# Kernel tuning notes

Hardware: AMD Instinct MI355X
Metric: run time of the kernel (lower is better)

## Reference

```python
import jax, jax.numpy as jnp
import numpy as np
import math

N_HEADS = 4
N_ITERS = 2  # SSFormer n=2; each loop iteration recomputes the same values (no feedback in the original code)
BN_EPS = 1e-5


def _attention(q, k, v):
    """SSTransformer: multi-head cross-attention over flattened spatial dims.
    q,k,v: [B, C, H, W] -> returns [B, C, L] with L = H*W.
    """
    b, c = q.shape[0], q.shape[1]
    L = q.shape[2] * q.shape[3]
    ch = c // N_HEADS
    scale = 1.0 / math.sqrt(math.sqrt(ch))
    qf = (q.reshape(b * N_HEADS, ch, L) * scale)
    kf = (k.reshape(b * N_HEADS, ch, L) * scale)
    vf = v.reshape(b * N_HEADS, ch, L)
    # weight: [B*H, t, s]
    w = jnp.einsum('bct,bcs->bts', qf, kf)
    w = jax.nn.softmax(w.astype(jnp.float32), axis=-1).astype(w.dtype)
    a = jnp.einsum('bts,bcs->bct', w, vf)
    return a.reshape(b, c, L)


def setup_inputs() -> dict:
    key = jax.random.key(0)
    k1, k2, k3, k4 = jax.random.split(key, 4)
    B, C, H, W = 8, 512, 32, 32
    c = jax.random.normal(k1, (B, C, H, W), dtype=jnp.float32)
    e = jax.random.normal(k2, (B, C, H, W), dtype=jnp.float32)
    conv_w = jax.random.normal(k3, (C, C, 1, 1), dtype=jnp.float32) / math.sqrt(C)
    conv_b = jax.random.normal(k4, (C,), dtype=jnp.float32) * 0.02
    bn_gamma = jnp.ones((C,), dtype=jnp.float32)
    bn_beta = jnp.zeros((C,), dtype=jnp.float32)
    return {"c": c, "e": e, "conv_w": conv_w, "conv_b": conv_b,
            "bn_gamma": bn_gamma, "bn_beta": bn_beta}


def reference(c, e, conv_w, conv_b, bn_gamma, bn_beta):
    bs, ch, h, w = c.shape
    L = h * w
    for _ in range(N_ITERS):
        _c = _attention(e, c, c)                       # [B, C, L]
        _e = _attention(_c.reshape(bs, ch, h, w), e, e)  # [B, C, L]
    _e = _e.reshape(bs, ch, h, w)
    # Proj: 1x1 conv + BatchNorm2d (training-mode batch stats) + Swish
    x = jnp.einsum('oc,bchw->bohw', conv_w.reshape(ch, ch), _e) + conv_b[None, :, None, None]
    mean = jnp.mean(x, axis=(0, 2, 3), keepdims=True)
    var = jnp.var(x, axis=(0, 2, 3), keepdims=True)
    xn = (x - mean) * jax.lax.rsqrt(var + BN_EPS)
    xn = xn * bn_gamma[None, :, None, None] + bn_beta[None, :, None, None]
    return xn * jax.nn.sigmoid(xn)
```

## Files before the change

### kernel.cpp

```cpp
#include <hip/hip_runtime.h>
#include <hip/hip_bf16.h>

typedef __attribute__((ext_vector_type(8))) short short8;
typedef __attribute__((ext_vector_type(4))) float floatx4;
typedef __attribute__((ext_vector_type(4))) float f32x4;
typedef __attribute__((ext_vector_type(16))) float f32x16;
typedef unsigned short u16;
typedef unsigned int u32;
typedef __attribute__((ext_vector_type(4))) unsigned int u32x4;
typedef __attribute__((ext_vector_type(8))) unsigned short ushort8;

#define LSEQ 1024
#define CHD  128
#define CEXP 0.12751744900425577f
#define THR_RAW 62.73318f

static __device__ __forceinline__ float b2f(u16 u) {
  union { u32 i; float f; } x; x.i = ((u32)u) << 16; return x.f;
}
static __device__ __forceinline__ u32 cvtpk(float a, float b) {
  u32 r;
  asm("v_cvt_pk_bf16_f32 %0, %1, %2" : "=v"(r) : "v"(a), "v"(b));
  return r;
}
static __device__ __forceinline__ void swap32(u32& a, u32& b) {
  asm("v_permlane32_swap_b32 %0, %1" : "+v"(a), "+v"(b));
}
static __device__ __forceinline__ short8 mk8(u32 a, u32 b, u32 c, u32 d) {
  union { u32x4 u; short8 s; } x;
  x.u[0] = a; x.u[1] = b; x.u[2] = c; x.u[3] = d;
  return x.s;
}
static __device__ __forceinline__ float exp2f_fast(float x) {
  float r;
  asm("v_exp_f32 %0, %1" : "=v"(r) : "v"(x));
  return r;
}
static __device__ __forceinline__ void gl_lds16(const void* g, void* l) {
  __builtin_amdgcn_global_load_lds((__attribute__((address_space(1))) const void*)g,
                                   (__attribute__((address_space(3))) void*)l, 16, 0, 0);
}
#define BARRIER() do { asm volatile("" ::: "memory"); __builtin_amdgcn_s_barrier(); asm volatile("" ::: "memory"); } while (0)
#define LGKMW()   do { asm volatile("s_waitcnt lgkmcnt(0)" ::: "memory"); } while (0)

__global__ __launch_bounds__(256) void k_prep(const float* __restrict__ cin,
                                              const float* __restrict__ ein,
                                              const float* __restrict__ Wf,
                                              u16* __restrict__ cV, u16* __restrict__ cT,
                                              u16* __restrict__ eV, u16* __restrict__ eT,
                                              u16* __restrict__ wb) {
  __shared__ u16 tile[32][72];
  int z = blockIdx.z;
  int tid = threadIdx.x;
  if (z >= 64) {
    int wblk = (z - 64) * 64 + blockIdx.y * 16 + blockIdx.x;
    int base = (wblk * 256 + tid) * 8;
    f32x4 a = *(const f32x4*)(Wf + base);
    f32x4 b = *(const f32x4*)(Wf + base + 4);
    u32x4 u;
    u[0] = cvtpk(a[0], a[1]); u[1] = cvtpk(a[2], a[3]);
    u[2] = cvtpk(b[0], b[1]); u[3] = cvtpk(b[2], b[3]);
    *(u32x4*)(wb + base) = u;
    return;
  }
  const float* in = (z < 32) ? cin : ein;
  u16* outV = (z < 32) ? cV : eV;
  u16* outT = (z < 32) ? cT : eT;
  int bh = z & 31, c0 = blockIdx.y * 32, s0 = blockIdx.x * 64;
  int cl = tid >> 3, sc = tid & 7;
  size_t off = ((size_t)bh * CHD + c0 + cl) * LSEQ + s0 + sc * 8;
  f32x4 a = *(const f32x4*)(in + off);
  f32x4 b = *(const f32x4*)(in + off + 4);
  u32x4 u;
  u[0] = cvtpk(a[0], a[1]); u[1] = cvtpk(a[2], a[3]);
  u[2] = cvtpk(b[0], b[1]); u[3] = cvtpk(b[2], b[3]);
  *(u32x4*)(outV + off) = u;
  *(u32x4*)&tile[cl][sc * 8] = u;
  __syncthreads();
  int sl = tid >> 2, cc = tid & 3;
  ushort8 v;
#pragma unroll
  for (int j = 0; j < 8; ++j) v[j] = tile[cc * 8 + j][sl];
  *(ushort8*)(outT + ((size_t)bh * LSEQ + s0 + sl) * CHD + c0 + cc * 8) = v;
}

__global__ __launch_bounds__(256, 2) void k_attn(const u16* __restrict__ eT,
                                                 const u16* __restrict__ cT,
                                                 const u16* __restrict__ cV,
                                                 const u16* __restrict__ eV,
                                                 u16* __restrict__ outT) {
  __shared__ char ldsbuf[66560];

  int bh = blockIdx.x, tt = blockIdx.y;
  int tid = threadIdx.x;
  int w = tid >> 6, lane = tid & 63;
  int tw = w & 1, sw = w >> 1;
  int ln = lane & 31, h = lane >> 5;
  int t0 = tt * 64 + tw * 32;

  float* bmbuf = (float*)(ldsbuf + 65536);
  float* lbuf  = (float*)(ldsbuf + 65536 + 512);

  auto stageK = [&](int buf, int sb, const char* kTb) {
#pragma unroll
    for (int it = 0; it < 4; ++it) {
      int bb = it * 4096 + tid * 16;
      int row = bb >> 8;
      int cb = (bb & 255) ^ ((row & 15) << 4);
      gl_lds16(kTb + (size_t)(sb * 64 + row) * 256 + cb, ldsbuf + buf * 16384 + bb);
    }
  };
  auto stageV = [&](int buf, int sb, const char* vb) {
#pragma unroll
    for (int it = 0; it < 4; ++it) {
      int bb = it * 4096 + tid * 16;
      int row = bb >> 7;
      int cb = (bb & 127) ^ ((row & 7) << 4);
      gl_lds16(vb + (size_t)row * 2048 + sb * 128 + cb, ldsbuf + 32768 + buf * 16384 + bb);
    }
  };

  short8 bq[8];
  f32x16 oacc[4];
  float m_r, l_r;
  int swz = (ln & 7) << 4;
  int kswz = (ln & 15) << 4;
  int krow = sw * 32 + ln;

  auto flash = [&](const char* kTb, const char* vb) {
    m_r = -1e30f; l_r = 0.f;
#pragma unroll
    for (int i = 0; i < 4; ++i)
#pragma unroll
      for (int r = 0; r < 16; ++r) oacc[i][r] = 0.f;

    stageK(0, 0, kTb); stageV(0, 0, vb);
    asm volatile("s_waitcnt vmcnt(0)" ::: "memory");
    BARRIER();

    for (int sb = 0; sb < 16; ++sb) {
      int cur = sb & 1;
      const char* K = ldsbuf + cur * 16384;
      const char* V = ldsbuf + 32768 + cur * 16384;
      f32x16 sa;
#pragma unroll
      for (int r = 0; r < 16; ++r) sa[r] = 0.f;

      if (sb < 15) stageK(cur ^ 1, sb + 1, kTb);
      short8 ka0 = *(const short8*)(K + krow * 256 + ((0  + h * 16) ^ kswz));
      short8 ka1 = *(const short8*)(K + krow * 256 + ((32 + h * 16) ^ kswz));
      short8 ka2 = *(const short8*)(K + krow * 256 + ((64 + h * 16) ^ kswz));
      short8 ka3 = *(const short8*)(K + krow * 256 + ((96 + h * 16) ^ kswz));
      BARRIER();
      __builtin_amdgcn_s_setprio(1);
      sa = __builtin_amdgcn_mfma_f32_32x32x16_bf16(ka0, bq[0], sa, 0, 0, 0);
      sa = __builtin_amdgcn_mfma_f32_32x32x16_bf16(ka1, bq[1], sa, 0, 0, 0);
      sa = __builtin_amdgcn_mfma_f32_32x32x16_bf16(ka2, bq[2], sa, 0, 0, 0);
      sa = __builtin_amdgcn_mfma_f32_32x32x16_bf16(ka3, bq[3], sa, 0, 0, 0);
      __builtin_amdgcn_s_setprio(0);
      BARRIER();

      if (sb < 15) stageV(cur ^ 1, sb + 1, vb);
      short8 kb0 = *(const short8*)(K + krow * 256 + ((128 + h * 16) ^ kswz));
      short8 kb1 = *(const short8*)(K + krow * 256 + ((160 + h * 16) ^ kswz));
      short8 kb2 = *(const short8*)(K + krow * 256 + ((192 + h * 16) ^ kswz));
      short8 kb3 = *(const short8*)(K + krow * 256 + ((224 + h * 16) ^ kswz));
      BARRIER();
      __builtin_amdgcn_s_setprio(1);
      sa = __builtin_amdgcn_mfma_f32_32x32x16_bf16(kb0, bq[4], sa, 0, 0, 0);
      sa = __builtin_amdgcn_mfma_f32_32x32x16_bf16(kb1, bq[5], sa, 0, 0, 0);
      sa = __builtin_amdgcn_mfma_f32_32x32x16_bf16(kb2, bq[6], sa, 0, 0, 0);
      sa = __builtin_amdgcn_mfma_f32_32x32x16_bf16(kb3, bq[7], sa, 0, 0, 0);
      __builtin_amdgcn_s_setprio(0);
      BARRIER();

      float bm = fmaxf(fmaxf(sa[0], sa[1]), fmaxf(sa[2], sa[3]));
      bm = fmaxf(bm, fmaxf(fmaxf(sa[4], sa[5]), fmaxf(sa[6], sa[7])));
      bm = fmaxf(bm, fmaxf(fmaxf(sa[8], sa[9]), fmaxf(sa[10], sa[11])));
      bm = fmaxf(bm, fmaxf(fmaxf(sa[12], sa[13]), fmaxf(sa[14], sa[15])));
      bm = fmaxf(bm, __shfl_xor(bm, 32));
      if (lane < 32) bmbuf[(tw * 2 + sw) * 32 + lane] = bm;
      LGKMW();
      BARRIER();
      bm = fmaxf(bm, bmbuf[(tw * 2 + (sw ^ 1)) * 32 + ln]);
      bool stay = __all(bm - m_r <= THR_RAW);
      if (!stay) {
        float mn = fmaxf(m_r, bm);
        float corr = exp2f_fast((m_r - mn) * CEXP);
        m_r = mn; l_r *= corr;
#pragma unroll
        for (int i = 0; i < 4; ++i)
#pragma unroll
          for (int r = 0; r < 16; ++r) oacc[i][r] *= corr;
      }
      float mnC = m_r * CEXP;
      float rs = 0.f;
#pragma unroll
      for (int r = 0; r < 16; ++r) {
        float p = exp2f_fast(__builtin_fmaf(sa[r], CEXP, -mnC));
        sa[r] = p; rs += p;
      }
      rs += __shfl_xor(rs, 32);
      l_r += rs;

      short8 bp0, bp1;
      {
        u32 w0 = cvtpk(sa[0], sa[1]),  w1 = cvtpk(sa[2], sa[3]);
        u32 w2 = cvtpk(sa[4], sa[5]),  w3 = cvtpk(sa[6], sa[7]);
        swap32(w0, w2); swap32(w1, w3);
        bp0 = mk8(w0, w1, w2, w3);
        u32 w4 = cvtpk(sa[8], sa[9]),  w5 = cvtpk(sa[10], sa[11]);
        u32 w6 = cvtpk(sa[12], sa[13]), w7 = cvtpk(sa[14], sa[15]);
        swap32(w4, w6); swap32(w5, w7);
        bp1 = mk8(w4, w5, w6, w7);
      }

      int vc0 = sw * 64 + h * 16;
      short8 va0 = *(const short8*)(V + (0  + ln) * 128 + (vc0 ^ swz));
      short8 va1 = *(const short8*)(V + (32 + ln) * 128 + (vc0 ^ swz));
      short8 va2 = *(const short8*)(V + (64 + ln) * 128 + (vc0 ^ swz));
      short8 va3 = *(const short8*)(V + (96 + ln) * 128 + (vc0 ^ swz));
      BARRIER();
      __builtin_amdgcn_s_setprio(1);
      oacc[0] = __builtin_amdgcn_mfma_f32_32x32x16_bf16(va0, bp0, oacc[0], 0, 0, 0);
      oacc[1] = __builtin_amdgcn_mfma_f32_32x32x16_bf16(va1, bp0, oacc[1], 0, 0, 0);
      oacc[2] = __builtin_amdgcn_mfma_f32_32x32x16_bf16(va2, bp0, oacc[2], 0, 0, 0);
      oacc[3] = __builtin_amdgcn_mfma_f32_32x32x16_bf16(va3, bp0, oacc[3], 0, 0, 0);
      __builtin_amdgcn_s_setprio(0);
      BARRIER();

      int vc1 = sw * 64 + 32 + h * 16;
      short8 vb0 = *(const short8*)(V + (0  + ln) * 128 + (vc1 ^ swz));
      short8 vb1 = *(const short8*)(V + (32 + ln) * 128 + (vc1 ^ swz));
      short8 vb2 = *(const short8*)(V + (64 + ln) * 128 + (vc1 ^ swz));
      short8 vb3 = *(const short8*)(V + (96 + ln) * 128 + (vc1 ^ swz));
      BARRIER();
      __builtin_amdgcn_s_setprio(1);
      oacc[0] = __builtin_amdgcn_mfma_f32_32x32x16_bf16(vb0, bp1, oacc[0], 0, 0, 0);
      oacc[1] = __builtin_amdgcn_mfma_f32_32x32x16_bf16(vb1, bp1, oacc[1], 0, 0, 0);
      oacc[2] = __builtin_amdgcn_mfma_f32_32x32x16_bf16(vb2, bp1, oacc[2], 0, 0, 0);
      oacc[3] = __builtin_amdgcn_mfma_f32_32x32x16_bf16(vb3, bp1, oacc[3], 0, 0, 0);
      __builtin_amdgcn_s_setprio(0);
      asm volatile("s_waitcnt vmcnt(0)" ::: "memory");
      BARRIER();
    }
  };

  auto merge_sw = [&]() {
    float* mb = (float*)(ldsbuf + 32768 + tw * 16384);
    if (sw == 1) {
#pragma unroll
      for (int i = 0; i < 4; ++i)
#pragma unroll
        for (int r = 0; r < 16; ++r) mb[(i * 16 + r) * 64 + lane] = oacc[i][r];
      if (lane < 32) lbuf[tw * 32 + lane] = l_r;
    }
    LGKMW();
    BARRIER();
    if (sw == 0) {
#pragma unroll
      for (int i = 0; i < 4; ++i)
#pragma unroll
        for (int r = 0; r < 16; ++r) oacc[i][r] += mb[(i * 16 + r) * 64 + lane];
      l_r += lbuf[tw * 32 + ln];
    }
  };

  const u16* qbase = eT + ((size_t)bh * LSEQ + t0 + ln) * CHD + h * 8;
#pragma unroll
  for (int k = 0; k < 8; ++k) bq[k] = *(const short8*)(qbase + k * 16);

  flash((const char*)(cT + (size_t)bh * LSEQ * CHD),
        (const char*)(cV + (size_t)bh * CHD * LSEQ));

  merge_sw();
  if (sw == 0) {
    float inv = 1.0f / l_r;
    char* qt = ldsbuf + tw * 8192;
#pragma unroll
    for (int m = 0; m < 4; ++m)
#pragma unroll
      for (int q = 0; q < 8; ++q) {
        u32 pk = cvtpk(oacc[m][2 * q] * inv, oacc[m][2 * q + 1] * inv);
        int c2 = m * 64 + 4 * (q & 1) + 16 * (q >> 1) + 8 * h;
        *(u32*)(qt + ln * 256 + (c2 ^ swz)) = pk;
      }
  }
  LGKMW();
  BARRIER();
  {
    const char* qt = ldsbuf + tw * 8192;
#pragma unroll
    for (int k = 0; k < 8; ++k)
      bq[k] = *(const short8*)(qt + ln * 256 + ((k * 32 + h * 16) ^ swz));
  }
  LGKMW();
  BARRIER();

  flash((const char*)(eT + (size_t)bh * LSEQ * CHD),
        (const char*)(eV + (size_t)bh * CHD * LSEQ));

  merge_sw();
  BARRIER();
  if (sw == 0) {
    float inv = 1.0f / l_r;
    char* ot = ldsbuf + tw * 8192;
#pragma unroll
    for (int m = 0; m < 4; ++m)
#pragma unroll
      for (int q = 0; q < 8; ++q) {
        u32 pk = cvtpk(oacc[m][2 * q] * inv, oacc[m][2 * q + 1] * inv);
        int c2 = m * 64 + 4 * (q & 1) + 16 * (q >> 1) + 8 * h;
        *(u32*)(ot + ln * 256 + (c2 ^ swz)) = pk;
      }
    asm volatile("" ::: "memory");
    u16* orow = outT + ((size_t)bh * LSEQ + t0 + ln) * CHD;
#pragma unroll
    for (int it = 0; it < 8; ++it) {
      int col = h * 128 + it * 16;
      ushort8 d = *(const ushort8*)(ot + ln * 256 + (col ^ swz));
      *(ushort8*)((char*)orow + col) = d;
    }
  }
}

__global__ __launch_bounds__(256) void k_proj(const u16* __restrict__ Wm,
                                              const u16* __restrict__ eT,
                                              const float* __restrict__ bias,
                                              u16* __restrict__ x,
                                              float* __restrict__ pstat) {
  __shared__ char lds[65536];
  int lt = blockIdx.x, ot = blockIdx.y;
  int b = lt >> 3;
  int l0b = (lt & 7) * 128;
  int o0 = ot * 128;
  int tid = threadIdx.x, w = tid >> 6, lane = tid & 63, lo = lane & 15, hi = lane >> 4;
  int wm = w >> 1, wn = w & 1;
  const char* Wb = (const char*)Wm;
  const char* eTb = (const char*)eT;

  auto stageA = [&](int buf, int kb) {
    char* dst = lds + buf * 16384;
#pragma unroll
    for (int it = 0; it < 4; ++it) {
      int bb = it * 4096 + tid * 16;
      int row = bb >> 7;
      int cb = (bb & 127) ^ ((row & 7) << 4);
      gl_lds16(Wb + (size_t)(o0 + row) * 1024 + kb * 128 + cb, dst + bb);
    }
  };
  auto stageB = [&](int buf, int kb) {
    char* dst = lds + 32768 + buf * 16384;
    int page = b * 4 + (kb >> 1);
    int choff = (kb & 1) * 128;
#pragma unroll
    for (int it = 0; it < 4; ++it) {
      int bb = it * 4096 + tid * 16;
      int row = bb >> 7;
      int cb = (bb & 127) ^ ((row & 7) << 4);
      gl_lds16(eTb + ((size_t)page * 1024 + l0b + row) * 256 + choff + cb, dst + bb);
    }
  };

  floatx4 acc[4][4];
#pragma unroll
  for (int i = 0; i < 4; ++i)
#pragma unroll
    for (int j = 0; j < 4; ++j) { acc[i][j][0]=0.f; acc[i][j][1]=0.f; acc[i][j][2]=0.f; acc[i][j][3]=0.f; }

  stageA(0, 0); stageB(0, 0);

  for (int kb = 0; kb < 8; ++kb) {
    int cur = kb & 1;
    __builtin_amdgcn_s_barrier();
    if (kb < 7) { stageA(cur ^ 1, kb + 1); stageB(cur ^ 1, kb + 1); }
    if (kb < 7) { asm volatile("s_waitcnt vmcnt(8)" ::: "memory"); }
    else        { asm volatile("s_waitcnt vmcnt(0)" ::: "memory"); }
    __builtin_amdgcn_s_barrier();
    const char* A = lds + cur * 16384;
    const char* B = lds + 32768 + cur * 16384;
#pragma unroll
    for (int kk = 0; kk < 2; ++kk) {
      short8 af[4], bf[4];
#pragma unroll
      for (int mi = 0; mi < 4; ++mi) {
        int row = wm * 64 + mi * 16 + lo;
        af[mi] = *(const short8*)(A + row * 128 + ((kk * 64 + hi * 16) ^ ((row & 7) << 4)));
      }
#pragma unroll
      for (int ni = 0; ni < 4; ++ni) {
        int row = wn * 64 + ni * 16 + lo;
        bf[ni] = *(const short8*)(B + row * 128 + ((kk * 64 + hi * 16) ^ ((row & 7) << 4)));
      }
      __builtin_amdgcn_s_setprio(1);
#pragma unroll
      for (int mi = 0; mi < 4; ++mi)
#pragma unroll
        for (int ni = 0; ni < 4; ++ni)
          acc[mi][ni] = __builtin_amdgcn_mfma_f32_16x16x32_bf16(af[mi], bf[ni], acc[mi][ni], 0, 0, 0);
      __builtin_amdgcn_s_setprio(0);
    }
  }

  int prow = lt * 2 + wn;
#pragma unroll
  for (int mi = 0; mi < 4; ++mi) {
#pragma unroll
    for (int r = 0; r < 4; ++r) {
      int o = o0 + wm * 64 + mi * 16 + hi * 4 + r;
      float bv = bias[o];
      float s = 0.f, q = 0.f;
#pragma unroll
      for (int ni = 0; ni < 4; ++ni) {
        float xv = acc[mi][ni][r] + bv;
        x[((size_t)b * 512 + o) * LSEQ + l0b + wn * 64 + ni * 16 + lo] = cvtpk(xv, xv) & 0xffff;
        s += xv; q += xv * xv;
      }
#pragma unroll
      for (int d = 1; d < 16; d <<= 1) { s += __shfl_xor(s, d); q += __shfl_xor(q, d); }
      if (lo == 0) {
        pstat[(size_t)prow * 512 + o] = s;
        pstat[65536 + (size_t)prow * 512 + o] = q;
      }
    }
  }
}

__global__ __launch_bounds__(256) void k_final(const u16* __restrict__ x,
                                               const float* __restrict__ pstat,
                                               const float* __restrict__ gamma,
                                               const float* __restrict__ beta,
                                               float* __restrict__ out) {
  __shared__ float sscale[2], sshift[2];
  int bid = blockIdx.x;
  int tid = threadIdx.x;
  if (tid < 128) {
    int k = tid >> 6;
    int chn = (bid * 2 + k) & 511;
    int l = tid & 63;
    float s = pstat[(size_t)l * 512 + chn] + pstat[(size_t)(l + 64) * 512 + chn];
    float q = pstat[65536 + (size_t)l * 512 + chn] + pstat[65536 + (size_t)(l + 64) * 512 + chn];
#pragma unroll
    for (int d = 1; d < 64; d <<= 1) { s += __shfl_xor(s, d); q += __shfl_xor(q, d); }
    if (l == 0) {
      const float invn = 1.0f / 8192.0f;
      float mean = s * invn;
      float var = q * invn - mean * mean;
      float rstd = rsqrtf(var + 1e-5f);
      float g = gamma[chn] * rstd;
      sscale[k] = g;
      sshift[k] = beta[chn] - mean * g;
    }
  }
  __syncthreads();
  int base = (bid * 256 + tid) * 8;
  int k2 = tid >> 7;
  float sc = sscale[k2], sh = sshift[k2];
  ushort8 vx = *(const ushort8*)(x + base);
  f32x4 o0, o1;
#pragma unroll
  for (int j = 0; j < 8; ++j) {
    float xn = b2f(vx[j]) * sc + sh;
    float sg = 1.0f / (1.0f + __expf(-xn));
    float r = xn * sg;
    if (j < 4) o0[j] = r; else o1[j - 4] = r;
  }
  *(f32x4*)(out + base) = o0;
  *(f32x4*)(out + base + 4) = o1;
}

extern "C" void kernel_launch(void* const* d_in, const int* in_sizes, int n_in,
                              void* d_out, int out_size, void* d_ws, size_t ws_size,
                              hipStream_t stream) {
  const float* c     = (const float*)d_in[0];
  const float* e     = (const float*)d_in[1];
  const float* Wf    = (const float*)d_in[2];
  const float* bias  = (const float*)d_in[3];
  const float* gamma = (const float*)d_in[4];
  const float* beta  = (const float*)d_in[5];
  float* outp = (float*)d_out;

  char* ws = (char*)d_ws;
  const size_t TB = (size_t)32 * 1024 * 128 * 2;
  u16* eT  = (u16*)(ws);
  u16* cT  = (u16*)(ws + TB);
  u16* cV  = (u16*)(ws + 2 * TB);
  u16* eV  = (u16*)(ws + 3 * TB);
  u16* xT  = (u16*)(ws + 4 * TB);
  u16* Wbf = (u16*)(ws + 5 * TB);
  float* pstat = (float*)(ws + 5 * TB + (2 << 20));
  u16* x   = (u16*)(ws + 6 * TB);

  dim3 tb(256);

  k_prep<<<dim3(16, 4, 66), tb, 0, stream>>>(c, e, Wf, cV, cT, eV, eT, Wbf);
  k_attn<<<dim3(32, 16), tb, 0, stream>>>(eT, cT, cV, eV, xT);
  k_proj<<<dim3(64, 4), tb, 0, stream>>>(Wbf, xT, bias, x, pstat);
  k_final<<<dim3(2048), tb, 0, stream>>>(x, pstat, gamma, beta, outp);
}
```

Baseline: 93.38 us.

## Load K directly into registers with prefetch and cut per-step barriers

K tiles now bypass LDS: each thread reads its own K fragments from global memory into registers and prefetches the next block's fragments while the current block is processed. V stays staged in LDS, with a partial vmcnt wait so the prefetched K loads can remain in flight. Several barriers around the QK and PV MFMA groups are removed and one is added before the merge. The cost is more VGPRs for the kc/kn arrays, which may hurt occupancy under launch_bounds(256,2), plus uncoalesced direct global reads of K.

```diff
diff --git a/kernel.cpp b/kernel.cpp
--- a/kernel.cpp
+++ b/kernel.cpp
@@ -101,15 +101,6 @@
   float* bmbuf = (float*)(ldsbuf + 65536);
   float* lbuf  = (float*)(ldsbuf + 65536 + 512);
 
-  auto stageK = [&](int buf, int sb, const char* kTb) {
-#pragma unroll
-    for (int it = 0; it < 4; ++it) {
-      int bb = it * 4096 + tid * 16;
-      int row = bb >> 8;
-      int cb = (bb & 255) ^ ((row & 15) << 4);
-      gl_lds16(kTb + (size_t)(sb * 64 + row) * 256 + cb, ldsbuf + buf * 16384 + bb);
-    }
-  };
   auto stageV = [&](int buf, int sb, const char* vb) {
 #pragma unroll
     for (int it = 0; it < 4; ++it) {
@@ -124,7 +115,6 @@
   f32x16 oacc[4];
   float m_r, l_r;
   int swz = (ln & 7) << 4;
-  int kswz = (ln & 15) << 4;
   int krow = sw * 32 + ln;
 
   auto flash = [&](const char* kTb, const char* vb) {
@@ -134,45 +124,36 @@
 #pragma unroll
       for (int r = 0; r < 16; ++r) oacc[i][r] = 0.f;
 
-    stageK(0, 0, kTb); stageV(0, 0, vb);
+    short8 kn[8], kc[8];
+    {
+      const char* kb = kTb + (size_t)krow * 256 + h * 16;
+#pragma unroll
+      for (int k = 0; k < 8; ++k) kn[k] = *(const short8*)(kb + k * 32);
+    }
+    stageV(0, 0, vb);
     asm volatile("s_waitcnt vmcnt(0)" ::: "memory");
     BARRIER();
 
     for (int sb = 0; sb < 16; ++sb) {
       int cur = sb & 1;
-      const char* K = ldsbuf + cur * 16384;
       const char* V = ldsbuf + 32768 + cur * 16384;
+
+#pragma unroll
+      for (int k = 0; k < 8; ++k) kc[k] = kn[k];
+
       f32x16 sa;
 #pragma unroll
       for (int r = 0; r < 16; ++r) sa[r] = 0.f;
-
-      if (sb < 15) stageK(cur ^ 1, sb + 1, kTb);
-      short8 ka0 = *(const short8*)(K + krow * 256 + ((0  + h * 16) ^ kswz));
-      short8 ka1 = *(const short8*)(K + krow * 256 + ((32 + h * 16) ^ kswz));
-      short8 ka2 = *(const short8*)(K + krow * 256 + ((64 + h * 16) ^ kswz));
-      short8 ka3 = *(const short8*)(K + krow * 256 + ((96 + h * 16) ^ kswz));
-      BARRIER();
       __builtin_amdgcn_s_setprio(1);
-      sa = __builtin_amdgcn_mfma_f32_32x32x16_bf16(ka0, bq[0], sa, 0, 0, 0);
-      sa = __builtin_amdgcn_mfma_f32_32x32x16_bf16(ka1, bq[1], sa, 0, 0, 0);
-      sa = __builtin_amdgcn_mfma_f32_32x32x16_bf16(ka2, bq[2], sa, 0, 0, 0);
-      sa = __builtin_amdgcn_mfma_f32_32x32x16_bf16(ka3, bq[3], sa, 0, 0, 0);
+      sa = __builtin_amdgcn_mfma_f32_32x32x16_bf16(kc[0], bq[0], sa, 0, 0, 0);
+      sa = __builtin_amdgcn_mfma_f32_32x32x16_bf16(kc[1], bq[1], sa, 0, 0, 0);
+      sa = __builtin_amdgcn_mfma_f32_32x32x16_bf16(kc[2], bq[2], sa, 0, 0, 0);
+      sa = __builtin_amdgcn_mfma_f32_32x32x16_bf16(kc[3], bq[3], sa, 0, 0, 0);
+      sa = __builtin_amdgcn_mfma_f32_32x32x16_bf16(kc[4], bq[4], sa, 0, 0, 0);
+      sa = __builtin_amdgcn_mfma_f32_32x32x16_bf16(kc[5], bq[5], sa, 0, 0, 0);
+      sa = __builtin_amdgcn_mfma_f32_32x32x16_bf16(kc[6], bq[6], sa, 0, 0, 0);
+      sa = __builtin_amdgcn_mfma_f32_32x32x16_bf16(kc[7], bq[7], sa, 0, 0, 0);
       __builtin_amdgcn_s_setprio(0);
-      BARRIER();
-
-      if (sb < 15) stageV(cur ^ 1, sb + 1, vb);
-      short8 kb0 = *(const short8*)(K + krow * 256 + ((128 + h * 16) ^ kswz));
-      short8 kb1 = *(const short8*)(K + krow * 256 + ((160 + h * 16) ^ kswz));
-      short8 kb2 = *(const short8*)(K + krow * 256 + ((192 + h * 16) ^ kswz));
-      short8 kb3 = *(const short8*)(K + krow * 256 + ((224 + h * 16) ^ kswz));
-      BARRIER();
-      __builtin_amdgcn_s_setprio(1);
-      sa = __builtin_amdgcn_mfma_f32_32x32x16_bf16(kb0, bq[4], sa, 0, 0, 0);
-      sa = __builtin_amdgcn_mfma_f32_32x32x16_bf16(kb1, bq[5], sa, 0, 0, 0);
-      sa = __builtin_amdgcn_mfma_f32_32x32x16_bf16(kb2, bq[6], sa, 0, 0, 0);
-      sa = __builtin_amdgcn_mfma_f32_32x32x16_bf16(kb3, bq[7], sa, 0, 0, 0);
-      __builtin_amdgcn_s_setprio(0);
-      BARRIER();
 
       float bm = fmaxf(fmaxf(sa[0], sa[1]), fmaxf(sa[2], sa[3]));
       bm = fmaxf(bm, fmaxf(fmaxf(sa[4], sa[5]), fmaxf(sa[6], sa[7])));
@@ -183,6 +164,14 @@
       LGKMW();
       BARRIER();
       bm = fmaxf(bm, bmbuf[(tw * 2 + (sw ^ 1)) * 32 + ln]);
+
+      if (sb < 15) {
+        const char* kb = kTb + (size_t)((sb + 1) * 64 + krow) * 256 + h * 16;
+#pragma unroll
+        for (int k = 0; k < 8; ++k) kn[k] = *(const short8*)(kb + k * 32);
+        stageV(cur ^ 1, sb + 1, vb);
+      }
+
       bool stay = __all(bm - m_r <= THR_RAW);
       if (!stay) {
         float mn = fmaxf(m_r, bm);
@@ -215,38 +204,37 @@
         bp1 = mk8(w4, w5, w6, w7);
       }
 
+      if (sb < 15) { asm volatile("s_waitcnt vmcnt(12)" ::: "memory"); }
+      else         { asm volatile("s_waitcnt vmcnt(0)" ::: "memory"); }
+      BARRIER();
+
       int vc0 = sw * 64 + h * 16;
-      short8 va0 = *(const short8*)(V + (0  + ln) * 128 + (vc0 ^ swz));
-      short8 va1 = *(const short8*)(V + (32 + ln) * 128 + (vc0 ^ swz));
-      short8 va2 = *(const short8*)(V + (64 + ln) * 128 + (vc0 ^ swz));
-      short8 va3 = *(const short8*)(V + (96 + ln) * 128 + (vc0 ^ swz));
-      BARRIER();
+      int vc1 = sw * 64 + 32 + h * 16;
       __builtin_amdgcn_s_setprio(1);
-      oacc[0] = __builtin_amdgcn_mfma_f32_32x32x16_bf16(va0, bp0, oacc[0], 0, 0, 0);
-      oacc[1] = __builtin_amdgcn_mfma_f32_32x32x16_bf16(va1, bp0, oacc[1], 0, 0, 0);
-      oacc[2] = __builtin_amdgcn_mfma_f32_32x32x16_bf16(va2, bp0, oacc[2], 0, 0, 0);
-      oacc[3] = __builtin_amdgcn_mfma_f32_32x32x16_bf16(va3, bp0, oacc[3], 0, 0, 0);
+      {
+        short8 va0 = *(const short8*)(V + (0  + ln) * 128 + (vc0 ^ swz));
+        short8 va1 = *(const short8*)(V + (32 + ln) * 128 + (vc0 ^ swz));
+        short8 va2 = *(const short8*)(V + (64 + ln) * 128 + (vc0 ^ swz));
+        short8 va3 = *(const short8*)(V + (96 + ln) * 128 + (vc0 ^ swz));
+        oacc[0] = __builtin_amdgcn_mfma_f32_32x32x16_bf16(va0, bp0, oacc[0], 0, 0, 0);
+        oacc[1] = __builtin_amdgcn_mfma_f32_32x32x16_bf16(va1, bp0, oacc[1], 0, 0, 0);
+        oacc[2] = __builtin_amdgcn_mfma_f32_32x32x16_bf16(va2, bp0, oacc[2], 0, 0, 0);
+        oacc[3] = __builtin_amdgcn_mfma_f32_32x32x16_bf16(va3, bp0, oacc[3], 0, 0, 0);
+        short8 vb0 = *(const short8*)(V + (0  + ln) * 128 + (vc1 ^ swz));
+        short8 vb1 = *(const short8*)(V + (32 + ln) * 128 + (vc1 ^ swz));
+        short8 vb2 = *(const short8*)(V + (64 + ln) * 128 + (vc1 ^ swz));
+        short8 vb3 = *(const short8*)(V + (96 + ln) * 128 + (vc1 ^ swz));
+        oacc[0] = __builtin_amdgcn_mfma_f32_32x32x16_bf16(vb0, bp1, oacc[0], 0, 0, 0);
+        oacc[1] = __builtin_amdgcn_mfma_f32_32x32x16_bf16(vb1, bp1, oacc[1], 0, 0, 0);
+        oacc[2] = __builtin_amdgcn_mfma_f32_32x32x16_bf16(vb2, bp1, oacc[2], 0, 0, 0);
+        oacc[3] = __builtin_amdgcn_mfma_f32_32x32x16_bf16(vb3, bp1, oacc[3], 0, 0, 0);
+      }
       __builtin_amdgcn_s_setprio(0);
-      BARRIER();
-
-      int vc1 = sw * 64 + 32 + h * 16;
-      short8 vb0 = *(const short8*)(V + (0  + ln) * 128 + (vc1 ^ swz));
-      short8 vb1 = *(const short8*)(V + (32 + ln) * 128 + (vc1 ^ swz));
-      short8 vb2 = *(const short8*)(V + (64 + ln) * 128 + (vc1 ^ swz));
-      short8 vb3 = *(const short8*)(V + (96 + ln) * 128 + (vc1 ^ swz));
-      BARRIER();
-      __builtin_amdgcn_s_setprio(1);
-      oacc[0] = __builtin_amdgcn_mfma_f32_32x32x16_bf16(vb0, bp1, oacc[0], 0, 0, 0);
-      oacc[1] = __builtin_amdgcn_mfma_f32_32x32x16_bf16(vb1, bp1, oacc[1], 0, 0, 0);
-      oacc[2] = __builtin_amdgcn_mfma_f32_32x32x16_bf16(vb2, bp1, oacc[2], 0, 0, 0);
-      oacc[3] = __builtin_amdgcn_mfma_f32_32x32x16_bf16(vb3, bp1, oacc[3], 0, 0, 0);
-      __builtin_amdgcn_s_setprio(0);
-      asm volatile("s_waitcnt vmcnt(0)" ::: "memory");
-      BARRIER();
     }
   };
 
   auto merge_sw = [&]() {
+    BARRIER();
     float* mb = (float*)(ldsbuf + 32768 + tw * 16384);
     if (sw == 1) {
 #pragma unroll
```

Result: slower. 111.5 us (+19.4%).
